# Performance work log

Hardware: AMD Instinct MI355X
Metric: run time of the kernel (lower is better)

## Reference

```python
import jax, jax.numpy as jnp
import numpy as np

B, N, K, C_IN, D = 4, 2048, 16, 480, 64
EPS = 1e-5


def _c1(x, w, b):
    # 1x1 Conv1d: x (B,C,N), w (O,C) -> (B,O,N)
    return jnp.einsum('oc,bcn->bon', w, x) + b[:, None]


def _c2(x, w, b):
    # 1x1 Conv2d: x (B,C,J,N), w (O,C) -> (B,O,J,N)
    return jnp.einsum('oc,bcjn->bojn', w, x) + b[:, None, None]


def _bn(x, g, b):
    # eval-mode BatchNorm2d with running_mean=0, running_var=1
    return x * (g / jnp.sqrt(1.0 + EPS))[:, None, None] + b[:, None, None]


def _mlp_res(x, w1, b1, w2, b2, ws, bs):
    return _c1(jax.nn.relu(_c1(x, w1, b1)), w2, b2) + _c1(x, ws, bs)


def _group(f, idx):
    # f (B,C,N), idx (B,K,N) int -> out[b,c,j,n] = f[b,c,idx[b,j,n]]  -> (B,C,K,N)
    return jax.vmap(lambda ff, ii: ff[:, ii])(f, idx)


def _knn_idx(xyz):
    # xyz (B,3,N) -> idx (B,K,N), excluding the self point (nearest neighbor)
    pts = xyz.transpose(0, 2, 1)  # (B,N,3)
    sq = jnp.sum(pts * pts, -1)
    d2 = sq[:, :, None] + sq[:, None, :] - 2.0 * jnp.einsum('bnd,bmd->bnm', pts, pts)
    _, idx = jax.lax.top_k(-d2, K + 1)  # (B,N,K+1), nearest first
    return idx.transpose(0, 2, 1)[:, 1:, :]  # drop self -> (B,K,N)


def _forward(idx, feature, xyz, bt1_w, bt1_b, bt2_w, bt2_b, bts_w, bts_b,
             q_w, q_b, k_w, k_b, v_w, v_b,
             fd1_w, fd1_b, fd_g, fd_bb, fd2_w, fd2_b,
             fg1_w, fg1_b, fg_g, fg_bb, fg2_w, fg2_b,
             at_w, at_b, m41_w, m41_b, m42_w, m42_b):
    x = _mlp_res(feature, bt1_w, bt1_b, bt2_w, bt2_b, bts_w, bts_b)  # (B,64,N)
    q = _c1(x, q_w, q_b)
    k = _c1(x, k_w, k_b)
    v = _c1(x, v_w, v_b)

    group_xyz = _group(xyz, idx)                       # (B,3,K,N)
    rel_xyz = xyz[:, :, None, :] - group_xyz           # (B,3,K,N)
    pos_enc = _c2(jax.nn.relu(_bn(_c2(rel_xyz, fd1_w, fd1_b), fd_g, fd_bb)), fd2_w, fd2_b)  # (B,64,K,N)

    k_local = _group(k, idx)                           # (B,64,K,N)
    v_local = _group(v, idx)
    qk_rel = q[:, :, None, :] - k_local
    attn = _c2(jax.nn.relu(_bn(_c2(qk_rel + pos_enc, fg1_w, fg1_b), fg_g, fg_bb)), fg2_w, fg2_b)  # (B,64,K,N)

    attn1 = attn.transpose(0, 1, 3, 2)                 # (B,64,N,K)
    # ConvTranspose2d(64,64,(4,1),(4,1)) with kernel==stride: out[b,o,4n+r,f] = sum_c x[b,c,n,f]*W[c,o,r] + bias[o]
    y = jnp.einsum('bcnf,cor->bonrf', attn1, at_w)
    y = y.reshape(y.shape[0], y.shape[1], -1, y.shape[4]) + at_b[None, :, None, None]  # (B,64,4N,K)
    attn = jax.nn.softmax(y, axis=1)

    value_rel = (v_local + pos_enc).transpose(0, 1, 3, 2)   # (B,64,N,K)
    value = jnp.repeat(value_rel, 4, axis=2)                # nearest upsample (4,1) -> (B,64,4N,K)

    res = jnp.einsum('bmnf,bmnf->bmn', attn, value)         # (B,64,4N)
    identity = jnp.repeat(x, 4, axis=2)                     # nearest upsample x4 -> (B,64,4N)
    res = res + identity
    completion = _c1(jax.nn.relu(_c1(res, m41_w, m41_b)), m42_w, m42_b)  # (B,3,4N)
    return completion, res


def setup_inputs() -> dict:
    key = jax.random.key(0)
    ks = jax.random.split(key, 24)
    i = iter(range(24))

    def w(shape):
        return (jax.random.normal(ks[next(i)], shape, dtype=jnp.float32) * 0.05)

    z = lambda n: jnp.zeros((n,), jnp.float32)
    o = lambda n: jnp.ones((n,), jnp.float32)
    return {
        'feature': jax.random.normal(ks[next(i)], (B, C_IN, N), dtype=jnp.float32),
        'xyz': jax.random.normal(ks[next(i)], (B, 3, N), dtype=jnp.float32),
        'bt1_w': w((D, C_IN)), 'bt1_b': z(D),
        'bt2_w': w((D, D)), 'bt2_b': z(D),
        'bts_w': w((D, C_IN)), 'bts_b': z(D),
        'q_w': w((D, D)), 'q_b': z(D),
        'k_w': w((D, D)), 'k_b': z(D),
        'v_w': w((D, D)), 'v_b': z(D),
        'fd1_w': w((D, 3)), 'fd1_b': z(D), 'fd_g': o(D), 'fd_bb': z(D),
        'fd2_w': w((D, D)), 'fd2_b': z(D),
        'fg1_w': w((4 * D, D)), 'fg1_b': z(4 * D), 'fg_g': o(4 * D), 'fg_bb': z(4 * D),
        'fg2_w': w((D, 4 * D)), 'fg2_b': z(D),
        'at_w': w((D, D, 4)), 'at_b': z(D),
        'm41_w': w((D, D)), 'm41_b': z(D),
        'm42_w': w((3, D)), 'm42_b': z(3),
    }


def reference(feature, xyz, bt1_w, bt1_b, bt2_w, bt2_b, bts_w, bts_b,
              q_w, q_b, k_w, k_b, v_w, v_b,
              fd1_w, fd1_b, fd_g, fd_bb, fd2_w, fd2_b,
              fg1_w, fg1_b, fg_g, fg_bb, fg2_w, fg2_b,
              at_w, at_b, m41_w, m41_b, m42_w, m42_b):
    idx = _knn_idx(xyz)
    return _forward(idx, feature, xyz, bt1_w, bt1_b, bt2_w, bt2_b, bts_w, bts_b,
                    q_w, q_b, k_w, k_b, v_w, v_b,
                    fd1_w, fd1_b, fd_g, fd_bb, fd2_w, fd2_b,
                    fg1_w, fg1_b, fg_g, fg_bb, fg2_w, fg2_b,
                    at_w, at_b, m41_w, m41_b, m42_w, m42_b)
```

## Files before the change

kernel.cpp:

```cpp
#include <hip/hip_runtime.h>

#define B_ 4
#define N_ 2048
#define K_ 16
#define CIN_ 480
#define UPN_ 8192
#define M_ (B_*N_*K_)
#define MX_ (B_*N_)
#define KCAP 448

typedef unsigned int u32;
typedef unsigned short u16;
typedef unsigned long long u64;
typedef __attribute__((ext_vector_type(8))) short short8;
typedef __attribute__((ext_vector_type(4))) float f32x4;

#define DEV static __device__ __forceinline__

DEV float b2f(u16 h){ return __uint_as_float(((u32)h)<<16); }
DEV u16 f2b(float f){
  u32 u = __float_as_uint(f);
  u32 r = u + 0x7fffu + ((u>>16)&1u);
  return (u16)(r>>16);
}
DEV u32 cvtpk(float a, float b){
  u32 r; asm("v_cvt_pk_bf16_f32 %0, %1, %2" : "=v"(r) : "v"(a), "v"(b));
  return r;
}
DEV u64 cvtpk4(float a, float b, float c, float d){
  return (u64)cvtpk(a,b) | ((u64)cvtpk(c,d)<<32);
}
DEV bool detect_bf(const void* fg){ return ((((const u32*)fg)[0]) & 0xFFFFu) == 0x3F80u; }
DEV float ld(const void* p, int i, bool bf){
  return bf ? b2f(((const u16*)p)[i]) : ((const float*)p)[i];
}
DEV u64 makekey(float d2, int m){
  u32 bits = __float_as_uint(d2);
  bits = (bits & 0x80000000u) ? ~bits : (bits | 0x80000000u);
  return ((u64)bits<<32) | (u32)m;
}
DEV int swz64 (int row, int colByte){ return row*128 + (colByte ^ ((row&7)<<4)); }
DEV int swz128(int row, int colByte){ return row*256 + (colByte ^ ((row&7)<<4)); }

__global__ __launch_bounds__(256) void convert_kernel(const void* __restrict__ xyz,
    const void* __restrict__ fg, float* __restrict__ fxyz)
{
  bool bf = detect_bf(fg);
  const int XT = B_*3*N_;
  for(int i = blockIdx.x*256+threadIdx.x; i < XT; i += gridDim.x*256)
    fxyz[i] = bf ? b2f(((const u16*)xyz)[i]) : ((const float*)xyz)[i];
}

__global__ __launch_bounds__(256) void transpose_kernel(const void* __restrict__ feature,
    const void* __restrict__ fg, u16* __restrict__ fxbT)
{
  __shared__ u16 s[32][34];
  bool bf = detect_bf(fg);
  int ntile = blockIdx.x, ctile = blockIdx.y, b = blockIdx.z;
  int tx = threadIdx.x & 31, ty = threadIdx.x >> 5;
  u64 base = (u64)b*CIN_*N_;
  #pragma unroll
  for(int r=0;r<4;r++){
    int c = ctile*32 + ty + r*8;
    int n = ntile*32 + tx;
    u64 i = base + (u64)c*N_ + n;
    s[ty + r*8][tx] = bf ? ((const u16*)feature)[i] : f2b(((const float*)feature)[i]);
  }
  __syncthreads();
  #pragma unroll
  for(int r=0;r<4;r++){
    int nl = ty + r*8;
    int n = ntile*32 + nl;
    fxbT[(u64)b*N_*CIN_ + (u64)n*CIN_ + ctile*32 + tx] = s[tx][nl];
  }
}

__global__ __launch_bounds__(256) void prep_kernel(
    const void* __restrict__ bt1_w, const void* __restrict__ bt1_b,
    const void* __restrict__ bt2_w, const void* __restrict__ bt2_b,
    const void* __restrict__ bts_w, const void* __restrict__ bts_b,
    const void* __restrict__ q_w, const void* __restrict__ q_b,
    const void* __restrict__ k_w, const void* __restrict__ k_b,
    const void* __restrict__ v_w, const void* __restrict__ v_b,
    const void* __restrict__ fd1_w, const void* __restrict__ fd1_b,
    const void* __restrict__ fd_g, const void* __restrict__ fd_bb,
    const void* __restrict__ fd2_w, const void* __restrict__ fd2_b,
    const void* __restrict__ fg1_w, const void* __restrict__ fg1_b,
    const void* __restrict__ fg_g, const void* __restrict__ fg_bb,
    const void* __restrict__ fg2_w, const void* __restrict__ fg2_b,
    const void* __restrict__ at_w, const void* __restrict__ at_b,
    const void* __restrict__ m41_w, const void* __restrict__ m41_b,
    const void* __restrict__ m42_w, const void* __restrict__ m42_b,
    float* __restrict__ W, u16* __restrict__ WB)
{
  int t = blockIdx.x*256 + threadIdx.x;
  bool bf = detect_bf(fd_g);
  const float inv = 0.9999950000374997f;
  if(t < 30720){ int c=t>>6, o=t&63; W[t] = ld(bt1_w,o*CIN_+c,bf); return; } t -= 30720;
  if(t < 30720){ int c=t>>6, o=t&63; W[30720+t] = ld(bts_w,o*CIN_+c,bf); return; } t -= 30720;
  if(t < 4096){ int c=t>>6, o=t&63; W[61440+t] = ld(bt2_w,o*64+c,bf); return; } t -= 4096;
  if(t < 4096){ int c=t>>6, o=t&63; W[65536+t] = ld(q_w,o*64+c,bf); return; } t -= 4096;
  if(t < 4096){ int c=t>>6, o=t&63; W[69632+t] = ld(k_w,o*64+c,bf); return; } t -= 4096;
  if(t < 4096){ int c=t>>6, o=t&63; W[73728+t] = ld(v_w,o*64+c,bf); return; } t -= 4096;
  if(t < 256){
    int o=t>>2, j=t&3; float s = ld(fd_g,o,bf)*inv;
    W[77824+t] = (j<3) ? s*ld(fd1_w,o*3+j,bf) : (s*ld(fd1_b,o,bf) + ld(fd_bb,o,bf));
    return;
  } t -= 256;
  if(t < 4096){ int o=t>>6, m=t&63; W[78080+t] = ld(fd2_w,m*64+o,bf); return; } t -= 4096;
  if(t < 16384){ int o=t>>6; float s=ld(fg_g,o,bf)*inv; W[82176+t] = s*ld(fg1_w,t,bf); return; } t -= 16384;
  if(t < 256){ float s=ld(fg_g,t,bf)*inv; W[98560+t] = s*ld(fg1_b,t,bf) + ld(fg_bb,t,bf); return; } t -= 256;
  if(t < 16384){ int o=t>>6, m=t&63; W[98816+t] = ld(fg2_w,m*256+o,bf); return; } t -= 16384;
  if(t < 16384){ int r=t>>12, rem=t&4095, o=rem>>6, c=rem&63;
                 W[115200+t] = ld(at_w,(c*64+o)*4+r,bf); return; } t -= 16384;
  if(t < 4096){ int m=t>>6, o=t&63; W[131584+t] = ld(m41_w,o*64+m,bf); return; } t -= 4096;
  if(t < 192){ W[135680+t] = ld(m42_w,t,bf); return; } t -= 192;
  if(t < 64){ W[135872+t] = ld(bt1_b,t,bf); return; } t -= 64;
  if(t < 64){ W[135936+t] = ld(bts_b,t,bf); return; } t -= 64;
  if(t < 64){ W[136000+t] = ld(bt2_b,t,bf); return; } t -= 64;
  if(t < 64){ W[136064+t] = ld(q_b,t,bf); return; } t -= 64;
  if(t < 64){ W[136128+t] = ld(k_b,t,bf); return; } t -= 64;
  if(t < 64){ W[136192+t] = ld(v_b,t,bf); return; } t -= 64;
  if(t < 64){ W[136256+t] = ld(fd2_b,t,bf); return; } t -= 64;
  if(t < 64){ W[136320+t] = ld(fg2_b,t,bf); return; } t -= 64;
  if(t < 64){ W[136384+t] = ld(at_b,t,bf); return; } t -= 64;
  if(t < 64){ W[136448+t] = ld(m41_b,t,bf); return; } t -= 64;
  if(t < 3){ W[136512+t] = ld(m42_b,t,bf); return; } t -= 3;
  if(t < 16384){ int o=t>>6; float s=ld(fg_g,o,bf)*inv; WB[t] = f2b(s*ld(fg1_w,t,bf)); return; } t -= 16384;
  if(t < 16384){ WB[16384+t] = f2b(ld(fg2_w,t,bf)); return; } t -= 16384;
  if(t < 16384){ int j=t>>6, c=t&63;
                 WB[32768+t] = f2b(ld(at_w,(c*64+(j&63))*4+(j>>6),bf)); return; } t -= 16384;
  if(t < 256){ W[136576+t] = ld(at_b,t&63,bf); return; } t -= 256;
  if(t < 4096){ WB[49152+t] = f2b(ld(fd2_w,t,bf)); return; } t -= 4096;
  if(t < 30720){ WB[53248+t] = f2b(ld(bt1_w,t,bf)); return; } t -= 30720;
  if(t < 30720){ WB[83968+t] = f2b(ld(bts_w,t,bf)); return; } t -= 30720;
  if(t < 4096){ WB[114688+t] = f2b(ld(bt2_w,t,bf)); return; } t -= 4096;
  if(t < 4096){ WB[118784+t] = f2b(ld(q_w,t,bf)); return; } t -= 4096;
  if(t < 4096){ WB[122880+t] = f2b(ld(k_w,t,bf)); return; } t -= 4096;
  if(t < 4096){ WB[126976+t] = f2b(ld(v_w,t,bf)); return; }
}

__global__ __launch_bounds__(256) void knn_kernel(const float* __restrict__ fxyz,
                                                  int* __restrict__ idx)
{
  __shared__ float px[N_], py[N_], pz[N_], sq[N_];
  __shared__ u64 sbuf[4][KCAP];
  __shared__ u64 smin[4][64];
  __shared__ int scnt[4][64];
  __shared__ u64 stau[4];
  int b = blockIdx.y;
  const float* xb = fxyz + (u64)b*3*N_;
  for(int i=threadIdx.x;i<N_;i+=256){
    float xx=xb[i], yy=xb[N_+i], zz=xb[2*N_+i];
    px[i]=xx; py[i]=yy; pz[i]=zz; sq[i]=xx*xx+yy*yy+zz*zz;
  }
  __syncthreads();
  int w = threadIdx.x>>6, l = threadIdx.x&63;
  int q = blockIdx.x*4 + w;
  float qx=px[q], qy=py[q], qz=pz[q], qs=sq[q];
  float d2c[32];
  u64 best=~0ull;
  #pragma unroll
  for(int j=0;j<32;j++){
    int m = l*32 + ((j+l)&31);
    float d2 = (qs+sq[m]) - 2.0f*(qx*px[m]+qy*py[m]+qz*pz[m]);
    d2c[j]=d2;
    u64 key = makekey(d2, m);
    best = key<best ? key : best;
  }
  smin[w][l]=best;
  __syncthreads();
  {
    int rank=0;
    for(int i=0;i<64;i++) rank += (smin[w][i] < best);
    if(rank==16) stau[w] = best;
  }
  __syncthreads();
  u64 tau = stau[w];
  int myc=0;
  #pragma unroll
  for(int j=0;j<32;j++){
    int m = l*32 + ((j+l)&31);
    myc += (makekey(d2c[j], m) <= tau);
  }
  scnt[w][l]=myc;
  __syncthreads();
  int off=0, tot=0;
  for(int i=0;i<64;i++){
    int c = scnt[w][i];
    tot += c;
    off += (i<l) ? c : 0;
  }
  #pragma unroll
  for(int j=0;j<32;j++){
    int m = l*32 + ((j+l)&31);
    u64 key = makekey(d2c[j], m);
    if(key<=tau && off<KCAP){ sbuf[w][off]=key; off++; }
  }
  __syncthreads();
  if(tot>KCAP) tot=KCAP;
  for(int p=l; p<tot; p+=64){
    u64 kk = sbuf[w][p];
    int rk=0;
    for(int i=0;i<tot;i++) rk += (sbuf[w][i] < kk);
    if(rk>=1 && rk<17) idx[(b*K_+(rk-1))*N_+q] = ((int)(kk & 0xffffffffu)) & (N_-1);
  }
}

__global__ __launch_bounds__(256,1) void prefix_mfma(const u16* __restrict__ A,
    const u16* __restrict__ Wg, const float* __restrict__ bg,
    const u16* __restrict__ Wbt2, const float* __restrict__ bbt2,
    const u16* __restrict__ Wqkv, const float* __restrict__ bqkv,
    float* __restrict__ x, float* __restrict__ qkvout)
{
  __shared__ alignas(16) unsigned char sh[65536];
  int tid=threadIdx.x, w=tid>>6, lane=tid&63;
  int lr=lane&15, lk=(lane>>4)*8, rq=(lane>>4)*4;
  u64 rbase=(u64)(blockIdx.x*4+w)*64;
  int lrow0 = w*64;

  f32x4 acc_h[4][4], acc_s[4][4];
  #pragma unroll
  for(int i=0;i<4;i++)
    #pragma unroll
    for(int j=0;j<4;j++){ acc_h[i][j]=(f32x4){0.f,0.f,0.f,0.f}; acc_s[i][j]=(f32x4){0.f,0.f,0.f,0.f}; }
  for(int kc=0;kc<CIN_;kc+=32){
    short8 af[4], wh[4], ws[4];
    #pragma unroll
    for(int ta=0;ta<4;ta++)
      af[ta] = *(const short8*)(A + (rbase+ta*16+lr)*CIN_ + kc + lk);
    #pragma unroll
    for(int tw=0;tw<4;tw++){
      wh[tw] = *(const short8*)(Wg + (u64)(tw*16+lr)*CIN_ + kc + lk);
      ws[tw] = *(const short8*)(Wg + (u64)(64+tw*16+lr)*CIN_ + kc + lk);
    }
    #pragma unroll
    for(int tw=0;tw<4;tw++)
      #pragma unroll
      for(int ta=0;ta<4;ta++){
        acc_h[tw][ta] = __builtin_amdgcn_mfma_f32_16x16x32_bf16(wh[tw], af[ta], acc_h[tw][ta], 0,0,0);
        acc_s[tw][ta] = __builtin_amdgcn_mfma_f32_16x16x32_bf16(ws[tw], af[ta], acc_s[tw][ta], 0,0,0);
      }
  }
  #pragma unroll
  for(int tw=0;tw<4;tw++){
    f32x4 b4 = *(const f32x4*)(bg + tw*16 + rq);
    #pragma unroll
    for(int ta=0;ta<4;ta++){
      int row = lrow0 + ta*16 + lr;
      *(u64*)(sh + swz64(row, (tw*16+rq)*2)) =
        cvtpk4(fmaxf(acc_h[tw][ta][0]+b4[0],0.f), fmaxf(acc_h[tw][ta][1]+b4[1],0.f),
               fmaxf(acc_h[tw][ta][2]+b4[2],0.f), fmaxf(acc_h[tw][ta][3]+b4[3],0.f));
    }
  }
  __syncthreads();
  {
    f32x4 acc_x[4][4];
    #pragma unroll
    for(int i=0;i<4;i++)
      #pragma unroll
      for(int j=0;j<4;j++) acc_x[i][j]=(f32x4){0.f,0.f,0.f,0.f};
    #pragma unroll
    for(int kc=0;kc<64;kc+=32){
      short8 wf[4], hf[4];
      #pragma unroll
      for(int tw=0;tw<4;tw++)
        wf[tw] = *(const short8*)(Wbt2 + (u64)(tw*16+lr)*64 + kc + lk);
      #pragma unroll
      for(int ta=0;ta<4;ta++)
        hf[ta] = *(const short8*)(sh + swz64(lrow0+ta*16+lr, (kc+lk)*2));
      #pragma unroll
      for(int tw=0;tw<4;tw++)
        #pragma unroll
        for(int ta=0;ta<4;ta++)
          acc_x[tw][ta] = __builtin_amdgcn_mfma_f32_16x16x32_bf16(wf[tw], hf[ta], acc_x[tw][ta], 0,0,0);
    }
    #pragma unroll
    for(int tw=0;tw<4;tw++){
      f32x4 bb = *(const f32x4*)(bbt2 + tw*16 + rq);
      f32x4 bs = *(const f32x4*)(bg + 64 + tw*16 + rq);
      #pragma unroll
      for(int ta=0;ta<4;ta++){
        int row = lrow0 + ta*16 + lr;
        f32x4 xv;
        #pragma unroll
        for(int reg=0;reg<4;reg++){
          float xsv = acc_s[tw][ta][reg] + bs[reg];
          xv[reg] = acc_x[tw][ta][reg] + bb[reg] + xsv;
        }
        *(f32x4*)(x + (rbase+ta*16+lr)*64 + tw*16 + rq) = xv;
        *(u64*)(sh + 32768 + swz64(row, (tw*16+rq)*2)) = cvtpk4(xv[0],xv[1],xv[2],xv[3]);
      }
    }
  }
  __syncthreads();
  #pragma unroll
  for(int g=0;g<3;g++){
    f32x4 acc[4][4];
    #pragma unroll
    for(int i=0;i<4;i++)
      #pragma unroll
      for(int j=0;j<4;j++) acc[i][j]=(f32x4){0.f,0.f,0.f,0.f};
    #pragma unroll
    for(int kc=0;kc<64;kc+=32){
      short8 wf[4], hf[4];
      #pragma unroll
      for(int tw=0;tw<4;tw++)
        wf[tw] = *(const short8*)(Wqkv + (u64)(g*64+tw*16+lr)*64 + kc + lk);
      #pragma unroll
      for(int ta=0;ta<4;ta++)
        hf[ta] = *(const short8*)(sh + 32768 + swz64(lrow0+ta*16+lr, (kc+lk)*2));
      #pragma unroll
      for(int tw=0;tw<4;tw++)
        #pragma unroll
        for(int ta=0;ta<4;ta++)
          acc[tw][ta] = __builtin_amdgcn_mfma_f32_16x16x32_bf16(wf[tw], hf[ta], acc[tw][ta], 0,0,0);
    }
    #pragma unroll
    for(int tw=0;tw<4;tw++){
      f32x4 bq = *(const f32x4*)(bqkv + g*64 + tw*16 + rq);
      #pragma unroll
      for(int ta=0;ta<4;ta++){
        f32x4 ov;
        #pragma unroll
        for(int reg=0;reg<4;reg++) ov[reg] = acc[tw][ta][reg] + bq[reg];
        *(f32x4*)(qkvout + (rbase+ta*16+lr)*192 + g*64 + tw*16 + rq) = ov;
      }
    }
  }
}

__global__ __launch_bounds__(256) void fused_chain(
    const int* __restrict__ idx, const float* __restrict__ fxyz,
    const float* __restrict__ qkv, const float* __restrict__ x,
    const float* __restrict__ fd1f,
    const u16* __restrict__ Wfd2, const float* __restrict__ bfd2,
    const u16* __restrict__ Wfg1, const float* __restrict__ bfg1,
    const u16* __restrict__ Wfg2, const float* __restrict__ bfg2,
    const u16* __restrict__ Wat,  const float* __restrict__ bat,
    const void* __restrict__ det, void* __restrict__ out)
{
  __shared__ alignas(16) unsigned char lds[32768];
  int tid = threadIdx.x;
  int w = tid>>6, lane = tid&63;
  int lr = lane&15, lk = (lane>>4)*8, rq = (lane>>4)*4;

  int erow = tid>>2, ecg = tid&3;
  int el = erow>>4, ef = erow&15;
  int bn_e = blockIdx.x*4 + el;
  int b_e = bn_e>>11, n_e = bn_e&(N_-1);
  int jn = idx[(b_e*K_+ef)*N_ + n_e] & (N_-1);

  {
    const float* xb = fxyz + (u64)b_e*3*N_;
    float rx = xb[n_e]      - xb[jn];
    float ry = xb[N_+n_e]   - xb[N_+jn];
    float rz = xb[2*N_+n_e] - xb[2*N_+jn];
    #pragma unroll
    for(int gg=0; gg<4; gg++){
      float tv[4];
      #pragma unroll
      for(int j=0;j<4;j++){
        f32x4 wv = *(const f32x4*)(fd1f + ((ecg*4+gg)*4+j)*4);
        tv[j] = fmaxf(wv[0]*rx + wv[1]*ry + wv[2]*rz + wv[3], 0.f);
      }
      *(u64*)(lds + swz64(erow, (ecg*4+gg)*8)) = cvtpk4(tv[0],tv[1],tv[2],tv[3]);
    }
  }
  __syncthreads();

  {
    f32x4 acc[4];
    #pragma unroll
    for(int i=0;i<4;i++) acc[i]=(f32x4){0.f,0.f,0.f,0.f};
    #pragma unroll
    for(int kc=0;kc<64;kc+=32){
      short8 wf = *(const short8*)(Wfd2 + (u64)(w*16+lr)*64 + kc + lk);
      #pragma unroll
      for(int ti=0;ti<4;ti++){
        short8 tf = *(const short8*)(lds + swz64(ti*16+lr, (kc+lk)*2));
        acc[ti] = __builtin_amdgcn_mfma_f32_16x16x32_bf16(wf, tf, acc[ti], 0,0,0);
      }
    }
    f32x4 b4 = *(const f32x4*)(bfd2 + w*16 + rq);
    #pragma unroll
    for(int ti=0;ti<4;ti++)
      *(u64*)(lds + 8192 + swz64(ti*16+lr, (w*16+rq)*2)) =
        cvtpk4(acc[ti][0]+b4[0], acc[ti][1]+b4[1], acc[ti][2]+b4[2], acc[ti][3]+b4[3]);
  }
  __syncthreads();

  {
    int mg = ecg*16;
    const float* qrow = qkv + (u64)(b_e*N_+n_e)*192 + mg;
    const float* krow = qkv + (u64)(b_e*N_+jn)*192 + 64 + mg;
    const float* vrow = qkv + (u64)(b_e*N_+jn)*192 + 128 + mg;
    #pragma unroll
    for(int g2=0; g2<4; g2++){
      f32x4 qv = *(const f32x4*)(qrow + g2*4);
      f32x4 kv = *(const f32x4*)(krow + g2*4);
      f32x4 vv = *(const f32x4*)(vrow + g2*4);
      int cb = (mg + g2*4)*2;
      u64 pw = *(const u64*)(lds + 8192 + swz64(erow, cb));
      float p0=b2f((u16)pw), p1=b2f((u16)(pw>>16)), p2=b2f((u16)(pw>>32)), p3=b2f((u16)(pw>>48));
      *(u64*)(lds + swz64(erow, cb)) =
        cvtpk4(qv[0]-kv[0]+p0, qv[1]-kv[1]+p1, qv[2]-kv[2]+p2, qv[3]-kv[3]+p3);
      *(u64*)(lds + 8192 + swz64(erow, cb)) =
        cvtpk4(vv[0]+p0, vv[1]+p1, vv[2]+p2, vv[3]+p3);
    }
  }
  __syncthreads();

  float vreg[16];
  #pragma unroll
  for(int f2=0; f2<16; f2++)
    vreg[f2] = b2f(*(const u16*)(lds + 8192 + swz64(w*16+f2, lane*2)));

  f32x4 gacc[4];
  #pragma unroll
  for(int i=0;i<4;i++) gacc[i]=(f32x4){0.f,0.f,0.f,0.f};
  #pragma unroll
  for(int half=0; half<2; half++){
    {
      f32x4 hacc[2][4];
      #pragma unroll
      for(int i=0;i<2;i++)
        #pragma unroll
        for(int j=0;j<4;j++) hacc[i][j]=(f32x4){0.f,0.f,0.f,0.f};
      #pragma unroll
      for(int kc=0;kc<64;kc+=32){
        short8 wf[2], af[4];
        #pragma unroll
        for(int ti=0;ti<2;ti++)
          wf[ti] = *(const short8*)(Wfg1 + (u64)(half*128 + w*32 + ti*16 + lr)*64 + kc + lk);
        #pragma unroll
        for(int tj=0;tj<4;tj++)
          af[tj] = *(const short8*)(lds + swz64(tj*16+lr, (kc+lk)*2));
        #pragma unroll
        for(int ti=0;ti<2;ti++)
          #pragma unroll
          for(int tj=0;tj<4;tj++)
            hacc[ti][tj] = __builtin_amdgcn_mfma_f32_16x16x32_bf16(wf[ti], af[tj], hacc[ti][tj], 0,0,0);
      }
      #pragma unroll
      for(int ti=0;ti<2;ti++){
        f32x4 b4 = *(const f32x4*)(bfg1 + half*128 + w*32 + ti*16 + rq);
        #pragma unroll
        for(int tj=0;tj<4;tj++){
          int row = tj*16 + lr;
          *(u64*)(lds + 16384 + swz128(row, (w*32+ti*16+rq)*2)) =
            cvtpk4(fmaxf(hacc[ti][tj][0]+b4[0],0.f), fmaxf(hacc[ti][tj][1]+b4[1],0.f),
                   fmaxf(hacc[ti][tj][2]+b4[2],0.f), fmaxf(hacc[ti][tj][3]+b4[3],0.f));
        }
      }
    }
    __syncthreads();
    #pragma unroll
    for(int kc=0;kc<128;kc+=32){
      short8 wf = *(const short8*)(Wfg2 + (u64)(w*16+lr)*256 + half*128 + kc + lk);
      #pragma unroll
      for(int tj=0;tj<4;tj++){
        short8 hf = *(const short8*)(lds + 16384 + swz128(tj*16+lr, (kc+lk)*2));
        gacc[tj] = __builtin_amdgcn_mfma_f32_16x16x32_bf16(wf, hf, gacc[tj], 0,0,0);
      }
    }
    __syncthreads();
  }

  {
    f32x4 b4 = *(const f32x4*)(bfg2 + w*16 + rq);
    #pragma unroll
    for(int tj=0;tj<4;tj++)
      *(u64*)(lds + swz64(tj*16+lr, (w*16+rq)*2)) =
        cvtpk4(gacc[tj][0]+b4[0], gacc[tj][1]+b4[1], gacc[tj][2]+b4[2], gacc[tj][3]+b4[3]);
  }
  __syncthreads();

  float aout[4];
  int srow = tid>>2, sub = tid&3;
  #pragma unroll
  for(int r=0;r<4;r++){
    {
      f32x4 acc[4];
      #pragma unroll
      for(int i=0;i<4;i++) acc[i]=(f32x4){0.f,0.f,0.f,0.f};
      #pragma unroll
      for(int kc=0;kc<64;kc+=32){
        short8 wf = *(const short8*)(Wat + (u64)(r*64 + w*16 + lr)*64 + kc + lk);
        #pragma unroll
        for(int tj=0;tj<4;tj++){
          short8 gf = *(const short8*)(lds + swz64(tj*16+lr, (kc+lk)*2));
          acc[tj] = __builtin_amdgcn_mfma_f32_16x16x32_bf16(wf, gf, acc[tj], 0,0,0);
        }
      }
      f32x4 b4 = *(const f32x4*)(bat + r*64 + w*16 + rq);
      #pragma unroll
      for(int tj=0;tj<4;tj++)
        *(u64*)(lds + 16384 + swz64(tj*16+lr, (w*16+rq)*2)) =
          cvtpk4(acc[tj][0]+b4[0], acc[tj][1]+b4[1], acc[tj][2]+b4[2], acc[tj][3]+b4[3]);
    }
    __syncthreads();
    {
      float yv[16];
      uint4 pk0 = *(const uint4*)(lds + 16384 + swz64(srow, sub*32));
      uint4 pk1 = *(const uint4*)(lds + 16384 + swz64(srow, sub*32 + 16));
      yv[0]=__uint_as_float(pk0.x<<16); yv[1]=__uint_as_float(pk0.x&0xffff0000u);
      yv[2]=__uint_as_float(pk0.y<<16); yv[3]=__uint_as_float(pk0.y&0xffff0000u);
      yv[4]=__uint_as_float(pk0.z<<16); yv[5]=__uint_as_float(pk0.z&0xffff0000u);
      yv[6]=__uint_as_float(pk0.w<<16); yv[7]=__uint_as_float(pk0.w&0xffff0000u);
      yv[8]=__uint_as_float(pk1.x<<16); yv[9]=__uint_as_float(pk1.x&0xffff0000u);
      yv[10]=__uint_as_float(pk1.y<<16); yv[11]=__uint_as_float(pk1.y&0xffff0000u);
      yv[12]=__uint_as_float(pk1.z<<16); yv[13]=__uint_as_float(pk1.z&0xffff0000u);
      yv[14]=__uint_as_float(pk1.w<<16); yv[15]=__uint_as_float(pk1.w&0xffff0000u);
      float mx = yv[0];
      #pragma unroll
      for(int m=1;m<16;m++) mx = fmaxf(mx, yv[m]);
      mx = fmaxf(mx, __shfl_xor(mx, 1));
      mx = fmaxf(mx, __shfl_xor(mx, 2));
      float sm = 0.f;
      #pragma unroll
      for(int m=0;m<16;m++){ float e = __expf(yv[m]-mx); yv[m]=e; sm+=e; }
      sm += __shfl_xor(sm, 1);
      sm += __shfl_xor(sm, 2);
      float rinv = 1.0f/sm;
      uint4 o0, o1;
      o0.x = cvtpk(yv[0]*rinv, yv[1]*rinv);  o0.y = cvtpk(yv[2]*rinv, yv[3]*rinv);
      o0.z = cvtpk(yv[4]*rinv, yv[5]*rinv);  o0.w = cvtpk(yv[6]*rinv, yv[7]*rinv);
      o1.x = cvtpk(yv[8]*rinv, yv[9]*rinv);  o1.y = cvtpk(yv[10]*rinv, yv[11]*rinv);
      o1.z = cvtpk(yv[12]*rinv, yv[13]*rinv); o1.w = cvtpk(yv[14]*rinv, yv[15]*rinv);
      *(uint4*)(lds + 8192 + swz64(srow, sub*32))      = o0;
      *(uint4*)(lds + 8192 + swz64(srow, sub*32 + 16)) = o1;
    }
    __syncthreads();
    {
      float a = 0.f;
      #pragma unroll
      for(int f2=0; f2<16; f2++)
        a += b2f(*(const u16*)(lds + 8192 + swz64(w*16+f2, lane*2))) * vreg[f2];
      aout[r] = a;
    }
  }

  int bn = blockIdx.x*4 + w;
  int b = bn>>11, n = bn&(N_-1);
  float xv = x[(u64)bn*64 + lane];
  u64 off = 98304 + ((u64)(b*64+lane))*UPN_ + (u64)n*4;
  if(detect_bf(det)){
    *(u64*)((u16*)out + off) = cvtpk4(aout[0]+xv, aout[1]+xv, aout[2]+xv, aout[3]+xv);
  } else {
    f32x4 pk = {aout[0]+xv, aout[1]+xv, aout[2]+xv, aout[3]+xv};
    *(f32x4*)((float*)out + off) = pk;
  }
}

__global__ __launch_bounds__(256) void comp_kernel(
  const float* __restrict__ m41T, const float* __restrict__ m41b,
  const float* __restrict__ m42f, const float* __restrict__ m42b,
  const void* __restrict__ det, void* __restrict__ out)
{
  int t = blockIdx.x*256 + threadIdx.x;
  int un = t & (UPN_-1);
  int b = t >> 13;
  bool bf = detect_bf(det);
  float acc[64];
  #pragma unroll
  for(int o=0;o<64;o++) acc[o] = m41b[o];
  if(bf){
    const u16* rr = (const u16*)out + 98304 + (u64)b*64*UPN_ + un;
    for(int c=0;c<64;c++){
      float rv = b2f(rr[(u64)c*UPN_]);
      const float* w = m41T + c*64;
      #pragma unroll
      for(int o=0;o<64;o++) acc[o] += w[o]*rv;
    }
  } else {
    const float* rr = (const float*)out + 98304 + (u64)b*64*UPN_ + un;
    for(int c=0;c<64;c++){
      float rv = rr[(u64)c*UPN_];
      const float* w = m41T + c*64;
      #pragma unroll
      for(int o=0;o<64;o++) acc[o] += w[o]*rv;
    }
  }
  float c0=m42b[0], c1=m42b[1], c2=m42b[2];
  #pragma unroll
  for(int o=0;o<64;o++){
    float hv = fmaxf(acc[o],0.f);
    c0 += m42f[o]*hv; c1 += m42f[64+o]*hv; c2 += m42f[128+o]*hv;
  }
  u64 base = (u64)b*3*UPN_ + un;
  if(bf){
    u16* cp = (u16*)out;
    cp[base]=f2b(c0); cp[base+UPN_]=f2b(c1); cp[base+2*UPN_]=f2b(c2);
  } else {
    float* cp = (float*)out;
    cp[base]=c0; cp[base+UPN_]=c1; cp[base+2*UPN_]=c2;
  }
}

extern "C" void kernel_launch(void* const* d_in, const int* in_sizes, int n_in,
                              void* d_out, int out_size, void* d_ws, size_t ws_size,
                              hipStream_t stream)
{
  (void)in_sizes; (void)n_in; (void)out_size; (void)ws_size;
  const void* feature=d_in[0];
  const void* xyz   =d_in[1];
  const void* bt1_w =d_in[2];  const void* bt1_b=d_in[3];
  const void* bt2_w =d_in[4];  const void* bt2_b=d_in[5];
  const void* bts_w =d_in[6];  const void* bts_b=d_in[7];
  const void* q_w   =d_in[8];  const void* q_b =d_in[9];
  const void* k_w   =d_in[10]; const void* k_b =d_in[11];
  const void* v_w   =d_in[12]; const void* v_b =d_in[13];
  const void* fd1_w =d_in[14]; const void* fd1_b=d_in[15];
  const void* fd_g  =d_in[16]; const void* fd_bb=d_in[17];
  const void* fd2_w =d_in[18]; const void* fd2_b=d_in[19];
  const void* fg1_w =d_in[20]; const void* fg1_b=d_in[21];
  const void* fg_g  =d_in[22]; const void* fg_bb=d_in[23];
  const void* fg2_w =d_in[24]; const void* fg2_b=d_in[25];
  const void* at_w  =d_in[26]; const void* at_b =d_in[27];
  const void* m41_w =d_in[28]; const void* m41_b=d_in[29];
  const void* m42_w =d_in[30]; const void* m42_b=d_in[31];

  char* ws=(char*)d_ws;
  float* W   =(float*)(ws);
  u16*  WB   =(u16*)  (ws + 589824);
  int*  idx  =(int*)  (ws + 851968);
  float* x   =(float*)(ws + 1376256);
  float* qkv =(float*)(ws + 3473408);
  u16*  fxbT =(u16*)  (ws + 114622464);
  float* fxyz=(float*)(ws + 122486784);

  const float* W_fd1f = W+77824;
  const float* W_fg1fb= W+98560;
  const float* W_m41T = W+131584;
  const float* W_m42  = W+135680;
  const float* Wb_g480= W+135872;
  const float* Wb_bt2 = W+136000;
  const float* Wb_qkv = W+136064;
  const float* Wb_fd2 = W+136256;
  const float* Wb_fg2 = W+136320;
  const float* Wb_m41 = W+136448;
  const float* Wb_m42 = W+136512;
  const float* W_atb256 = W+136576;
  const u16* WB_fg1  = WB;
  const u16* WB_fg2  = WB+16384;
  const u16* WB_at   = WB+32768;
  const u16* WB_fd2  = WB+49152;
  const u16* WB_g480 = WB+53248;
  const u16* WB_bt2  = WB+114688;
  const u16* WB_qkv  = WB+118784;

  convert_kernel<<<96,256,0,stream>>>(xyz, fd_g, fxyz);
  prep_kernel<<<1047,256,0,stream>>>(bt1_w,bt1_b,bt2_w,bt2_b,bts_w,bts_b,q_w,q_b,k_w,k_b,
      v_w,v_b,fd1_w,fd1_b,fd_g,fd_bb,fd2_w,fd2_b,fg1_w,fg1_b,fg_g,fg_bb,fg2_w,fg2_b,
      at_w,at_b,m41_w,m41_b,m42_w,m42_b,W,WB);
  transpose_kernel<<<dim3(64,15,4),256,0,stream>>>(feature, fd_g, fxbT);
  knn_kernel<<<dim3(N_/4,B_),256,0,stream>>>(fxyz, idx);
  prefix_mfma<<<MX_/256,256,0,stream>>>(fxbT, WB_g480, Wb_g480,
      WB_bt2, Wb_bt2, WB_qkv, Wb_qkv, x, qkv);
  fused_chain<<<B_*N_/4,256,0,stream>>>(idx, fxyz, qkv, x, W_fd1f,
      WB_fd2, Wb_fd2, WB_fg1, W_fg1fb, WB_fg2, Wb_fg2, WB_at, W_atb256, fd_g, d_out);
  comp_kernel<<<128,256,0,stream>>>(W_m41T, Wb_m41, W_m42, Wb_m42, fd_g, d_out);
}
```

Baseline: 286.7 us.

## Make MFMA chains wave-private to replace block barriers with per-wave LDS waits

Both prefix_mfma and fused_chain are restructured so each wave owns its rows end-to-end: one 16-row tile per wave, all output-channel tiles computed by that wave, in a private LDS slice. Block-wide __syncthreads is replaced by a per-wave lgkmcnt wait plus scheduling barrier. prefix_mfma now handles 16 rows per wave, launches four times as many blocks, uses much less LDS and drops the occupancy-1 launch bound. This targets barrier stalls and low occupancy, but each wave now reloads every weight tile itself, so there is less weight reuse per wave and more global or L2 traffic for weights.

```diff
diff --git a/kernel.cpp b/kernel.cpp
--- a/kernel.cpp
+++ b/kernel.cpp
@@ -16,6 +16,9 @@
 typedef __attribute__((ext_vector_type(4))) float f32x4;
 
 #define DEV static __device__ __forceinline__
+
+#define WAVE_WAIT() do{ asm volatile("s_waitcnt lgkmcnt(0)" ::: "memory"); \
+                        __builtin_amdgcn_sched_barrier(0); }while(0)
 
 DEV float b2f(u16 h){ return __uint_as_float(((u32)h)<<16); }
 DEV u16 f2b(float f){
@@ -207,125 +210,89 @@
   }
 }
 
-__global__ __launch_bounds__(256,1) void prefix_mfma(const u16* __restrict__ A,
+__global__ __launch_bounds__(256) void prefix_mfma(const u16* __restrict__ A,
     const u16* __restrict__ Wg, const float* __restrict__ bg,
     const u16* __restrict__ Wbt2, const float* __restrict__ bbt2,
     const u16* __restrict__ Wqkv, const float* __restrict__ bqkv,
     float* __restrict__ x, float* __restrict__ qkvout)
 {
-  __shared__ alignas(16) unsigned char sh[65536];
+  __shared__ alignas(16) unsigned char lds[16384];
   int tid=threadIdx.x, w=tid>>6, lane=tid&63;
   int lr=lane&15, lk=(lane>>4)*8, rq=(lane>>4)*4;
-  u64 rbase=(u64)(blockIdx.x*4+w)*64;
-  int lrow0 = w*64;
-
-  f32x4 acc_h[4][4], acc_s[4][4];
-  #pragma unroll
-  for(int i=0;i<4;i++)
-    #pragma unroll
-    for(int j=0;j<4;j++){ acc_h[i][j]=(f32x4){0.f,0.f,0.f,0.f}; acc_s[i][j]=(f32x4){0.f,0.f,0.f,0.f}; }
+  unsigned char* L = lds + w*4096;
+  u64 rbase=(u64)(blockIdx.x*4+w)*16;
+
+  f32x4 ah[4], as4[4];
+  #pragma unroll
+  for(int i=0;i<4;i++){ ah[i]=(f32x4){0.f,0.f,0.f,0.f}; as4[i]=(f32x4){0.f,0.f,0.f,0.f}; }
   for(int kc=0;kc<CIN_;kc+=32){
-    short8 af[4], wh[4], ws[4];
-    #pragma unroll
-    for(int ta=0;ta<4;ta++)
-      af[ta] = *(const short8*)(A + (rbase+ta*16+lr)*CIN_ + kc + lk);
-    #pragma unroll
-    for(int tw=0;tw<4;tw++){
-      wh[tw] = *(const short8*)(Wg + (u64)(tw*16+lr)*CIN_ + kc + lk);
-      ws[tw] = *(const short8*)(Wg + (u64)(64+tw*16+lr)*CIN_ + kc + lk);
-    }
-    #pragma unroll
-    for(int tw=0;tw<4;tw++)
-      #pragma unroll
-      for(int ta=0;ta<4;ta++){
-        acc_h[tw][ta] = __builtin_amdgcn_mfma_f32_16x16x32_bf16(wh[tw], af[ta], acc_h[tw][ta], 0,0,0);
-        acc_s[tw][ta] = __builtin_amdgcn_mfma_f32_16x16x32_bf16(ws[tw], af[ta], acc_s[tw][ta], 0,0,0);
-      }
-  }
-  #pragma unroll
-  for(int tw=0;tw<4;tw++){
-    f32x4 b4 = *(const f32x4*)(bg + tw*16 + rq);
-    #pragma unroll
-    for(int ta=0;ta<4;ta++){
-      int row = lrow0 + ta*16 + lr;
-      *(u64*)(sh + swz64(row, (tw*16+rq)*2)) =
-        cvtpk4(fmaxf(acc_h[tw][ta][0]+b4[0],0.f), fmaxf(acc_h[tw][ta][1]+b4[1],0.f),
-               fmaxf(acc_h[tw][ta][2]+b4[2],0.f), fmaxf(acc_h[tw][ta][3]+b4[3],0.f));
-    }
-  }
-  __syncthreads();
+    short8 af = *(const short8*)(A + (rbase+lr)*CIN_ + kc + lk);
+    #pragma unroll
+    for(int t=0;t<4;t++){
+      short8 wh = *(const short8*)(Wg + (u64)(t*16+lr)*CIN_ + kc + lk);
+      ah[t] = __builtin_amdgcn_mfma_f32_16x16x32_bf16(wh, af, ah[t], 0,0,0);
+    }
+    #pragma unroll
+    for(int t=0;t<4;t++){
+      short8 ws = *(const short8*)(Wg + (u64)(64+t*16+lr)*CIN_ + kc + lk);
+      as4[t] = __builtin_amdgcn_mfma_f32_16x16x32_bf16(ws, af, as4[t], 0,0,0);
+    }
+  }
+  #pragma unroll
+  for(int t=0;t<4;t++){
+    f32x4 b4 = *(const f32x4*)(bg + t*16 + rq);
+    *(u64*)(L + swz64(lr, (t*16+rq)*2)) =
+      cvtpk4(fmaxf(ah[t][0]+b4[0],0.f), fmaxf(ah[t][1]+b4[1],0.f),
+             fmaxf(ah[t][2]+b4[2],0.f), fmaxf(ah[t][3]+b4[3],0.f));
+  }
+  WAVE_WAIT();
   {
-    f32x4 acc_x[4][4];
-    #pragma unroll
-    for(int i=0;i<4;i++)
-      #pragma unroll
-      for(int j=0;j<4;j++) acc_x[i][j]=(f32x4){0.f,0.f,0.f,0.f};
+    f32x4 ax[4];
+    #pragma unroll
+    for(int i=0;i<4;i++) ax[i]=(f32x4){0.f,0.f,0.f,0.f};
     #pragma unroll
     for(int kc=0;kc<64;kc+=32){
-      short8 wf[4], hf[4];
-      #pragma unroll
-      for(int tw=0;tw<4;tw++)
-        wf[tw] = *(const short8*)(Wbt2 + (u64)(tw*16+lr)*64 + kc + lk);
-      #pragma unroll
-      for(int ta=0;ta<4;ta++)
-        hf[ta] = *(const short8*)(sh + swz64(lrow0+ta*16+lr, (kc+lk)*2));
-      #pragma unroll
-      for(int tw=0;tw<4;tw++)
-        #pragma unroll
-        for(int ta=0;ta<4;ta++)
-          acc_x[tw][ta] = __builtin_amdgcn_mfma_f32_16x16x32_bf16(wf[tw], hf[ta], acc_x[tw][ta], 0,0,0);
-    }
-    #pragma unroll
-    for(int tw=0;tw<4;tw++){
-      f32x4 bb = *(const f32x4*)(bbt2 + tw*16 + rq);
-      f32x4 bs = *(const f32x4*)(bg + 64 + tw*16 + rq);
-      #pragma unroll
-      for(int ta=0;ta<4;ta++){
-        int row = lrow0 + ta*16 + lr;
-        f32x4 xv;
-        #pragma unroll
-        for(int reg=0;reg<4;reg++){
-          float xsv = acc_s[tw][ta][reg] + bs[reg];
-          xv[reg] = acc_x[tw][ta][reg] + bb[reg] + xsv;
-        }
-        *(f32x4*)(x + (rbase+ta*16+lr)*64 + tw*16 + rq) = xv;
-        *(u64*)(sh + 32768 + swz64(row, (tw*16+rq)*2)) = cvtpk4(xv[0],xv[1],xv[2],xv[3]);
-      }
-    }
-  }
-  __syncthreads();
+      short8 hf = *(const short8*)(L + swz64(lr, (kc+lk)*2));
+      #pragma unroll
+      for(int t=0;t<4;t++){
+        short8 wf = *(const short8*)(Wbt2 + (u64)(t*16+lr)*64 + kc + lk);
+        ax[t] = __builtin_amdgcn_mfma_f32_16x16x32_bf16(wf, hf, ax[t], 0,0,0);
+      }
+    }
+    #pragma unroll
+    for(int t=0;t<4;t++){
+      f32x4 bb = *(const f32x4*)(bbt2 + t*16 + rq);
+      f32x4 bs = *(const f32x4*)(bg + 64 + t*16 + rq);
+      f32x4 xv;
+      #pragma unroll
+      for(int reg=0;reg<4;reg++)
+        xv[reg] = ax[t][reg] + bb[reg] + (as4[t][reg] + bs[reg]);
+      *(f32x4*)(x + (rbase+lr)*64 + t*16 + rq) = xv;
+      *(u64*)(L + 2048 + swz64(lr, (t*16+rq)*2)) = cvtpk4(xv[0],xv[1],xv[2],xv[3]);
+    }
+  }
+  WAVE_WAIT();
   #pragma unroll
   for(int g=0;g<3;g++){
-    f32x4 acc[4][4];
-    #pragma unroll
-    for(int i=0;i<4;i++)
-      #pragma unroll
-      for(int j=0;j<4;j++) acc[i][j]=(f32x4){0.f,0.f,0.f,0.f};
+    f32x4 aq[4];
+    #pragma unroll
+    for(int i=0;i<4;i++) aq[i]=(f32x4){0.f,0.f,0.f,0.f};
     #pragma unroll
     for(int kc=0;kc<64;kc+=32){
-      short8 wf[4], hf[4];
-      #pragma unroll
-      for(int tw=0;tw<4;tw++)
-        wf[tw] = *(const short8*)(Wqkv + (u64)(g*64+tw*16+lr)*64 + kc + lk);
-      #pragma unroll
-      for(int ta=0;ta<4;ta++)
-        hf[ta] = *(const short8*)(sh + 32768 + swz64(lrow0+ta*16+lr, (kc+lk)*2));
-      #pragma unroll
-      for(int tw=0;tw<4;tw++)
-        #pragma unroll
-        for(int ta=0;ta<4;ta++)
-          acc[tw][ta] = __builtin_amdgcn_mfma_f32_16x16x32_bf16(wf[tw], hf[ta], acc[tw][ta], 0,0,0);
-    }
-    #pragma unroll
-    for(int tw=0;tw<4;tw++){
-      f32x4 bq = *(const f32x4*)(bqkv + g*64 + tw*16 + rq);
-      #pragma unroll
-      for(int ta=0;ta<4;ta++){
-        f32x4 ov;
-        #pragma unroll
-        for(int reg=0;reg<4;reg++) ov[reg] = acc[tw][ta][reg] + bq[reg];
-        *(f32x4*)(qkvout + (rbase+ta*16+lr)*192 + g*64 + tw*16 + rq) = ov;
-      }
+      short8 hf = *(const short8*)(L + 2048 + swz64(lr, (kc+lk)*2));
+      #pragma unroll
+      for(int t=0;t<4;t++){
+        short8 wf = *(const short8*)(Wqkv + (u64)(g*64+t*16+lr)*64 + kc + lk);
+        aq[t] = __builtin_amdgcn_mfma_f32_16x16x32_bf16(wf, hf, aq[t], 0,0,0);
+      }
+    }
+    #pragma unroll
+    for(int t=0;t<4;t++){
+      f32x4 bq = *(const f32x4*)(bqkv + g*64 + t*16 + rq);
+      f32x4 ov;
+      #pragma unroll
+      for(int reg=0;reg<4;reg++) ov[reg] = aq[t][reg] + bq[reg];
+      *(f32x4*)(qkvout + (rbase+lr)*192 + g*64 + t*16 + rq) = ov;
     }
   }
 }
@@ -344,12 +311,12 @@
   int tid = threadIdx.x;
   int w = tid>>6, lane = tid&63;
   int lr = lane&15, lk = (lane>>4)*8, rq = (lane>>4)*4;
-
-  int erow = tid>>2, ecg = tid&3;
-  int el = erow>>4, ef = erow&15;
-  int bn_e = blockIdx.x*4 + el;
-  int b_e = bn_e>>11, n_e = bn_e&(N_-1);
-  int jn = idx[(b_e*K_+ef)*N_ + n_e] & (N_-1);
+  unsigned char* L = lds + w*8192;
+
+  int bn = blockIdx.x*4 + w;
+  int b_e = bn>>11, n_e = bn&(N_-1);
+  int f_a = lane>>2, ecg = lane&3;
+  int jn = idx[(b_e*K_+f_a)*N_ + n_e] & (N_-1);
 
   {
     const float* xb = fxyz + (u64)b_e*3*N_;
@@ -364,10 +331,10 @@
         f32x4 wv = *(const f32x4*)(fd1f + ((ecg*4+gg)*4+j)*4);
         tv[j] = fmaxf(wv[0]*rx + wv[1]*ry + wv[2]*rz + wv[3], 0.f);
       }
-      *(u64*)(lds + swz64(erow, (ecg*4+gg)*8)) = cvtpk4(tv[0],tv[1],tv[2],tv[3]);
-    }
-  }
-  __syncthreads();
+      *(u64*)(L + swz64(f_a, (ecg*4+gg)*8)) = cvtpk4(tv[0],tv[1],tv[2],tv[3]);
+    }
+  }
+  WAVE_WAIT();
 
   {
     f32x4 acc[4];
@@ -375,20 +342,21 @@
     for(int i=0;i<4;i++) acc[i]=(f32x4){0.f,0.f,0.f,0.f};
     #pragma unroll
     for(int kc=0;kc<64;kc+=32){
-      short8 wf = *(const short8*)(Wfd2 + (u64)(w*16+lr)*64 + kc + lk);
-      #pragma unroll
-      for(int ti=0;ti<4;ti++){
-        short8 tf = *(const short8*)(lds + swz64(ti*16+lr, (kc+lk)*2));
-        acc[ti] = __builtin_amdgcn_mfma_f32_16x16x32_bf16(wf, tf, acc[ti], 0,0,0);
-      }
-    }
-    f32x4 b4 = *(const f32x4*)(bfd2 + w*16 + rq);
-    #pragma unroll
-    for(int ti=0;ti<4;ti++)
-      *(u64*)(lds + 8192 + swz64(ti*16+lr, (w*16+rq)*2)) =
-        cvtpk4(acc[ti][0]+b4[0], acc[ti][1]+b4[1], acc[ti][2]+b4[2], acc[ti][3]+b4[3]);
-  }
-  __syncthreads();
+      short8 tf = *(const short8*)(L + swz64(lr, (kc+lk)*2));
+      #pragma unroll
+      for(int ct=0;ct<4;ct++){
+        short8 wf = *(const short8*)(Wfd2 + (u64)(ct*16+lr)*64 + kc + lk);
+        acc[ct] = __builtin_amdgcn_mfma_f32_16x16x32_bf16(wf, tf, acc[ct], 0,0,0);
+      }
+    }
+    #pragma unroll
+    for(int ct=0;ct<4;ct++){
+      f32x4 b4 = *(const f32x4*)(bfd2 + ct*16 + rq);
+      *(u64*)(L + 2048 + swz64(lr, (ct*16+rq)*2)) =
+        cvtpk4(acc[ct][0]+b4[0], acc[ct][1]+b4[1], acc[ct][2]+b4[2], acc[ct][3]+b4[3]);
+    }
+  }
+  WAVE_WAIT();
 
   {
     int mg = ecg*16;
@@ -401,20 +369,21 @@
       f32x4 kv = *(const f32x4*)(krow + g2*4);
       f32x4 vv = *(const f32x4*)(vrow + g2*4);
       int cb = (mg + g2*4)*2;
-      u64 pw = *(const u64*)(lds + 8192 + swz64(erow, cb));
+      u64 pw = *(const u64*)(L + 2048 + swz64(f_a, cb));
       float p0=b2f((u16)pw), p1=b2f((u16)(pw>>16)), p2=b2f((u16)(pw>>32)), p3=b2f((u16)(pw>>48));
-      *(u64*)(lds + swz64(erow, cb)) =
+      *(u64*)(L + swz64(f_a, cb)) =
         cvtpk4(qv[0]-kv[0]+p0, qv[1]-kv[1]+p1, qv[2]-kv[2]+p2, qv[3]-kv[3]+p3);
-      *(u64*)(lds + 8192 + swz64(erow, cb)) =
+      *(u64*)(L + 2048 + swz64(f_a, cb)) =
         cvtpk4(vv[0]+p0, vv[1]+p1, vv[2]+p2, vv[3]+p3);
     }
   }
-  __syncthreads();
+  WAVE_WAIT();
 
   float vreg[16];
   #pragma unroll
   for(int f2=0; f2<16; f2++)
-    vreg[f2] = b2f(*(const u16*)(lds + 8192 + swz64(w*16+f2, lane*2)));
+    vreg[f2] = b2f(*(const u16*)(L + 2048 + swz64(f2, lane*2)));
+  WAVE_WAIT();
 
   f32x4 gacc[4];
   #pragma unroll
@@ -422,62 +391,49 @@
   #pragma unroll
   for(int half=0; half<2; half++){
     {
-      f32x4 hacc[2][4];
-      #pragma unroll
-      for(int i=0;i<2;i++)
+      f32x4 hacc[8];
+      #pragma unroll
+      for(int i=0;i<8;i++) hacc[i]=(f32x4){0.f,0.f,0.f,0.f};
+      #pragma unroll
+      for(int kc=0;kc<64;kc+=32){
+        short8 af = *(const short8*)(L + swz64(lr, (kc+lk)*2));
         #pragma unroll
-        for(int j=0;j<4;j++) hacc[i][j]=(f32x4){0.f,0.f,0.f,0.f};
-      #pragma unroll
-      for(int kc=0;kc<64;kc+=32){
-        short8 wf[2], af[4];
-        #pragma unroll
-        for(int ti=0;ti<2;ti++)
-          wf[ti] = *(const short8*)(Wfg1 + (u64)(half*128 + w*32 + ti*16 + lr)*64 + kc + lk);
-        #pragma unroll
-        for(int tj=0;tj<4;tj++)
-          af[tj] = *(const short8*)(lds + swz64(tj*16+lr, (kc+lk)*2));
-        #pragma unroll
-        for(int ti=0;ti<2;ti++)
-          #pragma unroll
-          for(int tj=0;tj<4;tj++)
-            hacc[ti][tj] = __builtin_amdgcn_mfma_f32_16x16x32_bf16(wf[ti], af[tj], hacc[ti][tj], 0,0,0);
-      }
-      #pragma unroll
-      for(int ti=0;ti<2;ti++){
-        f32x4 b4 = *(const f32x4*)(bfg1 + half*128 + w*32 + ti*16 + rq);
-        #pragma unroll
-        for(int tj=0;tj<4;tj++){
-          int row = tj*16 + lr;
-          *(u64*)(lds + 16384 + swz128(row, (w*32+ti*16+rq)*2)) =
-            cvtpk4(fmaxf(hacc[ti][tj][0]+b4[0],0.f), fmaxf(hacc[ti][tj][1]+b4[1],0.f),
-                   fmaxf(hacc[ti][tj][2]+b4[2],0.f), fmaxf(hacc[ti][tj][3]+b4[3],0.f));
+        for(int ct=0;ct<8;ct++){
+          short8 wf = *(const short8*)(Wfg1 + (u64)(half*128 + ct*16 + lr)*64 + kc + lk);
+          hacc[ct] = __builtin_amdgcn_mfma_f32_16x16x32_bf16(wf, af, hacc[ct], 0,0,0);
         }
       }
-    }
-    __syncthreads();
+      #pragma unroll
+      for(int ct=0;ct<8;ct++){
+        f32x4 b4 = *(const f32x4*)(bfg1 + half*128 + ct*16 + rq);
+        *(u64*)(L + 4096 + swz128(lr, (ct*16+rq)*2)) =
+          cvtpk4(fmaxf(hacc[ct][0]+b4[0],0.f), fmaxf(hacc[ct][1]+b4[1],0.f),
+                 fmaxf(hacc[ct][2]+b4[2],0.f), fmaxf(hacc[ct][3]+b4[3],0.f));
+      }
+    }
+    WAVE_WAIT();
     #pragma unroll
     for(int kc=0;kc<128;kc+=32){
-      short8 wf = *(const short8*)(Wfg2 + (u64)(w*16+lr)*256 + half*128 + kc + lk);
-      #pragma unroll
-      for(int tj=0;tj<4;tj++){
-        short8 hf = *(const short8*)(lds + 16384 + swz128(tj*16+lr, (kc+lk)*2));
-        gacc[tj] = __builtin_amdgcn_mfma_f32_16x16x32_bf16(wf, hf, gacc[tj], 0,0,0);
-      }
-    }
-    __syncthreads();
-  }
-
-  {
-    f32x4 b4 = *(const f32x4*)(bfg2 + w*16 + rq);
-    #pragma unroll
-    for(int tj=0;tj<4;tj++)
-      *(u64*)(lds + swz64(tj*16+lr, (w*16+rq)*2)) =
-        cvtpk4(gacc[tj][0]+b4[0], gacc[tj][1]+b4[1], gacc[tj][2]+b4[2], gacc[tj][3]+b4[3]);
-  }
-  __syncthreads();
+      short8 hf = *(const short8*)(L + 4096 + swz128(lr, (kc+lk)*2));
+      #pragma unroll
+      for(int ct=0;ct<4;ct++){
+        short8 wf = *(const short8*)(Wfg2 + (u64)(ct*16+lr)*256 + half*128 + kc + lk);
+        gacc[ct] = __builtin_amdgcn_mfma_f32_16x16x32_bf16(wf, hf, gacc[ct], 0,0,0);
+      }
+    }
+    WAVE_WAIT();
+  }
+
+  #pragma unroll
+  for(int ct=0;ct<4;ct++){
+    f32x4 b4 = *(const f32x4*)(bfg2 + ct*16 + rq);
+    *(u64*)(L + swz64(lr, (ct*16+rq)*2)) =
+      cvtpk4(gacc[ct][0]+b4[0], gacc[ct][1]+b4[1], gacc[ct][2]+b4[2], gacc[ct][3]+b4[3]);
+  }
+  WAVE_WAIT();
 
   float aout[4];
-  int srow = tid>>2, sub = tid&3;
+  int sub = lane&3;
   #pragma unroll
   for(int r=0;r<4;r++){
     {
@@ -486,24 +442,25 @@
       for(int i=0;i<4;i++) acc[i]=(f32x4){0.f,0.f,0.f,0.f};
       #pragma unroll
       for(int kc=0;kc<64;kc+=32){
-        short8 wf = *(const short8*)(Wat + (u64)(r*64 + w*16 + lr)*64 + kc + lk);
+        short8 gf = *(const short8*)(L + swz64(lr, (kc+lk)*2));
         #pragma unroll
-        for(int tj=0;tj<4;tj++){
-          short8 gf = *(const short8*)(lds + swz64(tj*16+lr, (kc+lk)*2));
-          acc[tj] = __builtin_amdgcn_mfma_f32_16x16x32_bf16(wf, gf, acc[tj], 0,0,0);
+        for(int ct=0;ct<4;ct++){
+          short8 wf = *(const short8*)(Wat + (u64)(r*64 + ct*16 + lr)*64 + kc + lk);
+          acc[ct] = __builtin_amdgcn_mfma_f32_16x16x32_bf16(wf, gf, acc[ct], 0,0,0);
         }
       }
-      f32x4 b4 = *(const f32x4*)(bat + r*64 + w*16 + rq);
-      #pragma unroll
-      for(int tj=0;tj<4;tj++)
-        *(u64*)(lds + 16384 + swz64(tj*16+lr, (w*16+rq)*2)) =
-          cvtpk4(acc[tj][0]+b4[0], acc[tj][1]+b4[1], acc[tj][2]+b4[2], acc[tj][3]+b4[3]);
-    }
-    __syncthreads();
+      #pragma unroll
+      for(int ct=0;ct<4;ct++){
+        f32x4 b4 = *(const f32x4*)(bat + r*64 + ct*16 + rq);
+        *(u64*)(L + 4096 + swz64(lr, (ct*16+rq)*2)) =
+          cvtpk4(acc[ct][0]+b4[0], acc[ct][1]+b4[1], acc[ct][2]+b4[2], acc[ct][3]+b4[3]);
+      }
+    }
+    WAVE_WAIT();
     {
       float yv[16];
-      uint4 pk0 = *(const uint4*)(lds + 16384 + swz64(srow, sub*32));
-      uint4 pk1 = *(const uint4*)(lds + 16384 + swz64(srow, sub*32 + 16));
+      uint4 pk0 = *(const uint4*)(L + 4096 + swz64(f_a, sub*32));
+      uint4 pk1 = *(const uint4*)(L + 4096 + swz64(f_a, sub*32 + 16));
       yv[0]=__uint_as_float(pk0.x<<16); yv[1]=__uint_as_float(pk0.x&0xffff0000u);
       yv[2]=__uint_as_float(pk0.y<<16); yv[3]=__uint_as_float(pk0.y&0xffff0000u);
       yv[4]=__uint_as_float(pk0.z<<16); yv[5]=__uint_as_float(pk0.z&0xffff0000u);
@@ -528,20 +485,20 @@
       o0.z = cvtpk(yv[4]*rinv, yv[5]*rinv);  o0.w = cvtpk(yv[6]*rinv, yv[7]*rinv);
       o1.x = cvtpk(yv[8]*rinv, yv[9]*rinv);  o1.y = cvtpk(yv[10]*rinv, yv[11]*rinv);
       o1.z = cvtpk(yv[12]*rinv, yv[13]*rinv); o1.w = cvtpk(yv[14]*rinv, yv[15]*rinv);
-      *(uint4*)(lds + 8192 + swz64(srow, sub*32))      = o0;
-      *(uint4*)(lds + 8192 + swz64(srow, sub*32 + 16)) = o1;
-    }
-    __syncthreads();
+      *(uint4*)(L + 2048 + swz64(f_a, sub*32))      = o0;
+      *(uint4*)(L + 2048 + swz64(f_a, sub*32 + 16)) = o1;
+    }
+    WAVE_WAIT();
     {
       float a = 0.f;
       #pragma unroll
       for(int f2=0; f2<16; f2++)
-        a += b2f(*(const u16*)(lds + 8192 + swz64(w*16+f2, lane*2))) * vreg[f2];
+        a += b2f(*(const u16*)(L + 2048 + swz64(f2, lane*2))) * vreg[f2];
       aout[r] = a;
     }
-  }
-
-  int bn = blockIdx.x*4 + w;
+    WAVE_WAIT();
+  }
+
   int b = bn>>11, n = bn&(N_-1);
   float xv = x[(u64)bn*64 + lane];
   u64 off = 98304 + ((u64)(b*64+lane))*UPN_ + (u64)n*4;
@@ -656,7 +613,7 @@
       at_w,at_b,m41_w,m41_b,m42_w,m42_b,W,WB);
   transpose_kernel<<<dim3(64,15,4),256,0,stream>>>(feature, fd_g, fxbT);
   knn_kernel<<<dim3(N_/4,B_),256,0,stream>>>(fxyz, idx);
-  prefix_mfma<<<MX_/256,256,0,stream>>>(fxbT, WB_g480, Wb_g480,
+  prefix_mfma<<<MX_/64,256,0,stream>>>(fxbT, WB_g480, Wb_g480,
       WB_bt2, Wb_bt2, WB_qkv, Wb_qkv, x, qkv);
   fused_chain<<<B_*N_/4,256,0,stream>>>(idx, fxyz, qkv, x, W_fd1f,
       WB_fd2, Wb_fd2, WB_fg1, W_fg1fb, WB_fg2, Wb_fg2, WB_at, W_atb256, fd_g, d_out);
```

After: 353.2 us. 23.2% more time.
